# Performance work log

Hardware: AMD Instinct MI355X
Metric: run time of the kernel (lower is better)

## Reference

```python
import jax, jax.numpy as jnp
import numpy as np

N, D, H, O = 8192, 1024, 4096, 1024   # tokens, input_dim, hidden_dim, output_dim
E, K, CAP = 8, 2, 4096                # num_experts, top_k, expert_capacity


def setup_inputs() -> dict:
    key = jax.random.key(0)
    ks = jax.random.split(key, 7)
    sd = 0.02
    return {
        "x": jax.random.normal(ks[0], (N, D), jnp.float32),
        "gate_W": jax.random.normal(ks[1], (E, D), jnp.float32) * sd,
        "gate_b": jnp.zeros((E,), jnp.float32),
        "W1": jax.random.normal(ks[2], (E, D, H), jnp.float32) * sd,
        "b1": jnp.zeros((E, H), jnp.float32),
        "W2": jax.random.normal(ks[3], (E, H, O), jnp.float32) * sd,
        "b2": jnp.zeros((E, O), jnp.float32),
    }


def reference(x, gate_W, gate_b, W1, b1, W2, b2):
    n = x.shape[0]
    # --- gating ---
    logits = x @ gate_W.T + gate_b                      # [N, E]
    probs = jax.nn.softmax(logits, axis=-1)
    topk_probs, topk_idx = jax.lax.top_k(probs, K)      # [N, K]

    # --- aux losses (training mode) ---
    importance = probs.sum(0)                           # [E]
    importance_loss = jnp.var(importance, ddof=1) / (E ** 2)  # torch.var is unbiased
    mask = jnp.zeros((n, E), bool).at[jnp.arange(n)[:, None], topk_idx].set(True)
    routing_probs = probs * mask
    expert_usage = mask.astype(probs.dtype).mean(0)
    routing_weights = routing_probs.mean(0)
    load_balance_loss = E * (expert_usage * routing_weights).sum()
    aux_loss = importance_loss + load_balance_loss

    # --- capacity-constrained dispatch (matches torch flat-order truncation) ---
    flat_idx = topk_idx.reshape(-1)                     # [N*K] expert of each assignment
    flat_probs = topk_probs.reshape(-1)                 # [N*K]
    sample_idx = jnp.repeat(jnp.arange(n), K)           # [N*K] token of each assignment
    onehot = (flat_idx[:, None] == jnp.arange(E)[None, :])          # [N*K, E]
    pos = (jnp.cumsum(onehot, axis=0) * onehot).sum(-1) - 1         # slot within expert
    keep = pos < CAP                                    # torch keeps first CAP in flat order
    slot = jnp.where(keep, flat_idx * CAP + pos, E * CAP)           # dropped -> padding slot
    disp_sample = jnp.zeros(E * CAP + 1, jnp.int32).at[slot].set(sample_idx.astype(jnp.int32))
    disp_w = jnp.zeros(E * CAP + 1, x.dtype).at[slot].set(flat_probs)
    tok = disp_sample[: E * CAP]                        # [E*CAP] source token per slot

    # --- grouped expert MLP ---
    xe = x[tok].reshape(E, CAP, D)                      # gather into [E, CAP, D]
    h = jax.nn.relu(jnp.einsum('ecd,edh->ech', xe, W1) + b1[:, None, :])
    y = jnp.einsum('ech,eho->eco', h, W2) + b2[:, None, :]

    # --- weighted scatter-combine (unfilled slots have weight 0) ---
    w = disp_w[: E * CAP].reshape(E, CAP, 1)
    out = jnp.zeros((n, O), x.dtype).at[tok].add((y * w).reshape(E * CAP, O))
    return out, aux_loss
```

## Files before the change

kernel.cpp:

```cpp
#include <hip/hip_runtime.h>

#define N_TOK 8192
#define DIM   1024
#define HID   4096
#define OUTD  1024
#define NE    8
#define CAPE  4096

typedef _Float16 f16;
typedef f16  f16x8 __attribute__((ext_vector_type(8)));
typedef f16  f16x4 __attribute__((ext_vector_type(4)));
typedef float f32x4 __attribute__((ext_vector_type(4)));

__device__ __forceinline__ void gload16(const void* g, void* l) {
  __builtin_amdgcn_global_load_lds(
      (const __attribute__((address_space(1))) void*)g,
      (__attribute__((address_space(3))) void*)l, 16, 0, 0);
}

__global__ void zero_ctrl(int* counts) {
  if (threadIdx.x < NE) counts[threadIdx.x] = 0;
}

__global__ __launch_bounds__(256) void zero_out(float4* __restrict__ p) {
  p[(size_t)blockIdx.x * 256 + threadIdx.x] = float4{0.f, 0.f, 0.f, 0.f};
}

__global__ __launch_bounds__(256) void transpose_cvt(
    const float* __restrict__ in, f16* __restrict__ out, int R, int C, int g0) {
  __shared__ float tile[32][33];
  const int ez = blockIdx.z;
  const int r0 = blockIdx.y * 32;
  const int c0 = blockIdx.x * 32;
  const float* ip = in  + (size_t)(g0 + ez) * R * C;
  f16*         op = out + (size_t)ez * R * C;
  const int tx = threadIdx.x;
  const int ty = threadIdx.y;
#pragma unroll
  for (int k = 0; k < 4; ++k) {
    int r = ty + k * 8;
    tile[r][tx] = ip[(size_t)(r0 + r) * C + c0 + tx];
  }
  __syncthreads();
#pragma unroll
  for (int k = 0; k < 4; ++k) {
    int r = ty + k * 8;
    op[(size_t)(c0 + r) * R + r0 + tx] = (f16)tile[tx][r];
  }
}

__global__ __launch_bounds__(256) void gate_kernel(
    const float* __restrict__ x, const float* __restrict__ gW,
    const float* __restrict__ gb, int* __restrict__ counts,
    int* __restrict__ tk_e, int* __restrict__ tk_pos, float* __restrict__ tk_w,
    float* __restrict__ blockImp, float* __restrict__ blockRw) {
  const int tid  = threadIdx.x;
  const int wave = tid >> 6;
  const int lane = tid & 63;
  const int t    = blockIdx.x * 4 + wave;

  float acc[NE];
#pragma unroll
  for (int e = 0; e < NE; ++e) acc[e] = 0.f;

  const float* xr = x + (size_t)t * DIM;
  for (int d = lane; d < DIM; d += 64) {
    float xv = xr[d];
#pragma unroll
    for (int e = 0; e < NE; ++e) acc[e] += xv * gW[e * DIM + d];
  }
#pragma unroll
  for (int off = 32; off; off >>= 1) {
#pragma unroll
    for (int e = 0; e < NE; ++e) acc[e] += __shfl_xor(acc[e], off);
  }
  float p[NE];
  float mx = -1e30f;
#pragma unroll
  for (int e = 0; e < NE; ++e) { p[e] = acc[e] + gb[e]; mx = fmaxf(mx, p[e]); }
  float s = 0.f;
#pragma unroll
  for (int e = 0; e < NE; ++e) { p[e] = expf(p[e] - mx); s += p[e]; }
  float inv = 1.f / s;
#pragma unroll
  for (int e = 0; e < NE; ++e) p[e] *= inv;

  int e0 = 0;
#pragma unroll
  for (int e = 1; e < NE; ++e) if (p[e] > p[e0]) e0 = e;
  int e1 = (e0 == 0) ? 1 : 0;
#pragma unroll
  for (int e = 0; e < NE; ++e) if (e != e0 && p[e] > p[e1]) e1 = e;

  __shared__ float simp[4][NE];
  __shared__ float srw[4][NE];
  if (lane == 0) {
    int p0 = atomicAdd(&counts[e0], 1);
    int p1 = atomicAdd(&counts[e1], 1);
    tk_e[t * 2]     = e0;  tk_e[t * 2 + 1]   = e1;
    tk_pos[t * 2]   = p0;  tk_pos[t * 2 + 1] = p1;
    tk_w[t * 2]     = p[e0]; tk_w[t * 2 + 1] = p[e1];
#pragma unroll
    for (int e = 0; e < NE; ++e) {
      simp[wave][e] = p[e];
      srw[wave][e]  = (e == e0) ? p[e0] : ((e == e1) ? p[e1] : 0.f);
    }
  }
  __syncthreads();
  if (tid < NE) {
    float si = 0.f, sr = 0.f;
#pragma unroll
    for (int w = 0; w < 4; ++w) { si += simp[w][tid]; sr += srw[w][tid]; }
    blockImp[blockIdx.x * NE + tid] = si;
    blockRw[blockIdx.x * NE + tid]  = sr;
  }
}

__global__ __launch_bounds__(256) void gather_x(
    const float* __restrict__ x, const int* __restrict__ tk_e,
    const int* __restrict__ tk_pos, const float* __restrict__ tk_w,
    f16* __restrict__ Xg, int* __restrict__ slot_tok,
    float* __restrict__ slot_w, int g0, int G) {
  const int i   = blockIdx.x;
  const int e   = tk_e[i];
  if (e < g0 || e >= g0 + G) return;
  const int pos = tk_pos[i];
  if (pos >= CAPE) return;
  const int t = i >> 1;
  if (threadIdx.x == 0) {
    slot_tok[e * CAPE + pos] = t;
    slot_w[e * CAPE + pos]   = tk_w[i];
  }
  const float4* src = (const float4*)(x + (size_t)t * DIM);
  f16* dst = Xg + ((size_t)((e - g0) * CAPE + pos)) * DIM;
  const int c = threadIdx.x;
  float4 v = src[c];
  f16x4 h;
  h.x = (f16)v.x; h.y = (f16)v.y; h.z = (f16)v.z; h.w = (f16)v.w;
  *(f16x4*)(dst + c * 4) = h;
}

__global__ __launch_bounds__(256) void gemm1_kernel(
    const f16* __restrict__ Xg, const f16* __restrict__ W1t,
    const float* __restrict__ b1, f16* __restrict__ Hb,
    const int* __restrict__ counts, int g0) {
  const int ez  = blockIdx.z;
  const int e   = g0 + ez;
  int cnt = counts[e]; if (cnt > CAPE) cnt = CAPE;
  const int brow = blockIdx.y;
  const int bcol = blockIdx.x;
  if (brow * 128 >= cnt) return;

  __shared__ f16 As[128 * 32];
  __shared__ f16 Bs[128 * 32];

  const int tid  = threadIdx.x;
  const int wave = tid >> 6, lane = tid & 63;
  const int wr = wave >> 1, wc = wave & 1;
  const int srow = tid >> 2;
  const int scol = (tid & 3) * 8;

  const f16* Ab = Xg  + ((size_t)ez * CAPE + brow * 128) * DIM;
  const f16* Bb = W1t + ((size_t)ez * HID  + bcol * 128) * DIM;

  f32x4 acc[4][4];
#pragma unroll
  for (int i = 0; i < 4; ++i)
#pragma unroll
    for (int j = 0; j < 4; ++j) acc[i][j] = (f32x4){0.f, 0.f, 0.f, 0.f};

  const int fr = lane & 15, fk = (lane >> 4) * 8;

  for (int kt = 0; kt < DIM / 32; ++kt) {
    const f16* Ak = Ab + kt * 32;
    const f16* Bk = Bb + kt * 32;
    gload16(Ak + (size_t)srow * DIM + scol,        As + wave * 512);
    gload16(Ak + (size_t)(srow + 64) * DIM + scol, As + 2048 + wave * 512);
    gload16(Bk + (size_t)srow * DIM + scol,        Bs + wave * 512);
    gload16(Bk + (size_t)(srow + 64) * DIM + scol, Bs + 2048 + wave * 512);
    __syncthreads();
    f16x8 af[4], bf[4];
#pragma unroll
    for (int i = 0; i < 4; ++i)
      af[i] = *(const f16x8*)&As[(wr * 64 + i * 16 + fr) * 32 + fk];
#pragma unroll
    for (int j = 0; j < 4; ++j)
      bf[j] = *(const f16x8*)&Bs[(wc * 64 + j * 16 + fr) * 32 + fk];
#pragma unroll
    for (int i = 0; i < 4; ++i)
#pragma unroll
      for (int j = 0; j < 4; ++j)
        acc[i][j] = __builtin_amdgcn_mfma_f32_16x16x32_f16(af[i], bf[j], acc[i][j], 0, 0, 0);
    __syncthreads();
  }

  const int rbase = (lane >> 4) * 4;
  const int crow0 = brow * 128 + wr * 64;
  const int ccol0 = bcol * 128 + wc * 64;
  f16* Cb = Hb + (size_t)ez * CAPE * HID;
#pragma unroll
  for (int j = 0; j < 4; ++j) {
    int col = ccol0 + j * 16 + fr;
    float bias = b1[e * HID + col];
#pragma unroll
    for (int i = 0; i < 4; ++i) {
#pragma unroll
      for (int r = 0; r < 4; ++r) {
        int row = crow0 + i * 16 + rbase + r;
        float v = acc[i][j][r] + bias;
        Cb[(size_t)row * HID + col] = (f16)(v > 0.f ? v : 0.f);
      }
    }
  }
}

__global__ __launch_bounds__(256) void gemm2_kernel(
    const f16* __restrict__ Hb, const f16* __restrict__ W2t,
    const float* __restrict__ b2, float* __restrict__ out,
    const int* __restrict__ slot_tok, const float* __restrict__ slot_w,
    const int* __restrict__ counts, int g0) {
  const int ez  = blockIdx.z;
  const int e   = g0 + ez;
  int cnt = counts[e]; if (cnt > CAPE) cnt = CAPE;
  const int brow = blockIdx.y;
  const int bcol = blockIdx.x;
  if (brow * 128 >= cnt) return;

  __shared__ f16 As[128 * 32];
  __shared__ f16 Bs[128 * 32];

  const int tid  = threadIdx.x;
  const int wave = tid >> 6, lane = tid & 63;
  const int wr = wave >> 1, wc = wave & 1;
  const int srow = tid >> 2;
  const int scol = (tid & 3) * 8;

  const f16* Ab = Hb  + ((size_t)ez * CAPE + brow * 128) * HID;
  const f16* Bb = W2t + ((size_t)ez * OUTD + bcol * 128) * HID;

  f32x4 acc[4][4];
#pragma unroll
  for (int i = 0; i < 4; ++i)
#pragma unroll
    for (int j = 0; j < 4; ++j) acc[i][j] = (f32x4){0.f, 0.f, 0.f, 0.f};

  const int fr = lane & 15, fk = (lane >> 4) * 8;

  for (int kt = 0; kt < HID / 32; ++kt) {
    const f16* Ak = Ab + kt * 32;
    const f16* Bk = Bb + kt * 32;
    gload16(Ak + (size_t)srow * HID + scol,        As + wave * 512);
    gload16(Ak + (size_t)(srow + 64) * HID + scol, As + 2048 + wave * 512);
    gload16(Bk + (size_t)srow * HID + scol,        Bs + wave * 512);
    gload16(Bk + (size_t)(srow + 64) * HID + scol, Bs + 2048 + wave * 512);
    __syncthreads();
    f16x8 af[4], bf[4];
#pragma unroll
    for (int i = 0; i < 4; ++i)
      af[i] = *(const f16x8*)&As[(wr * 64 + i * 16 + fr) * 32 + fk];
#pragma unroll
    for (int j = 0; j < 4; ++j)
      bf[j] = *(const f16x8*)&Bs[(wc * 64 + j * 16 + fr) * 32 + fk];
#pragma unroll
    for (int i = 0; i < 4; ++i)
#pragma unroll
      for (int j = 0; j < 4; ++j)
        acc[i][j] = __builtin_amdgcn_mfma_f32_16x16x32_f16(af[i], bf[j], acc[i][j], 0, 0, 0);
    __syncthreads();
  }

  const int rbase = (lane >> 4) * 4;
  const int crow0 = brow * 128 + wr * 64;
  const int ccol0 = bcol * 128 + wc * 64;

  int   tok[4][4];
  float twt[4][4];
#pragma unroll
  for (int i = 0; i < 4; ++i) {
#pragma unroll
    for (int r = 0; r < 4; ++r) {
      int row = crow0 + i * 16 + rbase + r;
      if (row < cnt) {
        tok[i][r] = slot_tok[(size_t)e * CAPE + row];
        twt[i][r] = slot_w[(size_t)e * CAPE + row];
      } else {
        tok[i][r] = -1;
        twt[i][r] = 0.f;
      }
    }
  }

#pragma unroll
  for (int j = 0; j < 4; ++j) {
    int col = ccol0 + j * 16 + fr;
    float bias = b2[e * OUTD + col];
#pragma unroll
    for (int i = 0; i < 4; ++i) {
#pragma unroll
      for (int r = 0; r < 4; ++r) {
        if (tok[i][r] >= 0) {
          float v = twt[i][r] * (acc[i][j][r] + bias);
          atomicAdd(&out[(size_t)tok[i][r] * OUTD + col], v);
        }
      }
    }
  }
}

__global__ void aux_kernel(const float* __restrict__ blockImp,
                           const float* __restrict__ blockRw,
                           const int* __restrict__ counts,
                           float* __restrict__ out_aux) {
  const int lane = threadIdx.x;
  const int e   = lane >> 3;
  const int idx = lane & 7;
  double imp = 0.0, rw = 0.0;
  for (int b = idx; b < N_TOK / 4; b += 8) {
    imp += (double)blockImp[b * NE + e];
    rw  += (double)blockRw[b * NE + e];
  }
#pragma unroll
  for (int off = 1; off < 8; off <<= 1) {
    imp += __shfl_xor(imp, off);
    rw  += __shfl_xor(rw, off);
  }
  __shared__ double simp[NE], srw[NE];
  if (idx == 0) { simp[e] = imp; srw[e] = rw; }
  __syncthreads();
  if (lane == 0) {
    double mean = 0.0;
    for (int i = 0; i < NE; ++i) mean += simp[i];
    mean /= NE;
    double var = 0.0;
    for (int i = 0; i < NE; ++i) { double d = simp[i] - mean; var += d * d; }
    var /= (NE - 1);
    double il = var / (NE * NE);
    double lb = 0.0;
    for (int i = 0; i < NE; ++i)
      lb += ((double)counts[i] / N_TOK) * (srw[i] / N_TOK);
    lb *= NE;
    out_aux[0] = (float)(il + lb);
  }
}

extern "C" void kernel_launch(void* const* d_in, const int* in_sizes, int n_in,
                              void* d_out, int out_size, void* d_ws, size_t ws_size,
                              hipStream_t stream) {
  const float* x   = (const float*)d_in[0];
  const float* gW  = (const float*)d_in[1];
  const float* gb  = (const float*)d_in[2];
  const float* W1  = (const float*)d_in[3];
  const float* b1  = (const float*)d_in[4];
  const float* W2  = (const float*)d_in[5];
  const float* b2  = (const float*)d_in[6];
  float* out = (float*)d_out;

  char* ws = (char*)d_ws;
  size_t off = 0;
  int* counts   = (int*)(ws + off); off += 256;
  int* tk_e     = (int*)(ws + off); off += (size_t)N_TOK * 2 * 4;
  int* tk_pos   = (int*)(ws + off); off += (size_t)N_TOK * 2 * 4;
  float* tk_w   = (float*)(ws + off); off += (size_t)N_TOK * 2 * 4;
  int* slot_tok = (int*)(ws + off); off += (size_t)NE * CAPE * 4;
  float* slot_w = (float*)(ws + off); off += (size_t)NE * CAPE * 4;
  float* blockImp = (float*)(ws + off); off += (size_t)(N_TOK / 4) * NE * 4;
  float* blockRw  = (float*)(ws + off); off += (size_t)(N_TOK / 4) * NE * 4;
  off = (off + 255) & ~(size_t)255;

  const size_t w1t_pe = (size_t)HID  * DIM * 2;
  const size_t w2t_pe = (size_t)OUTD * HID * 2;
  const size_t xg_pe  = (size_t)CAPE * DIM * 2;
  const size_t hb_pe  = (size_t)CAPE * HID * 2;
  const size_t per_e  = w1t_pe + w2t_pe + xg_pe + hb_pe;

  int G = 1;
  for (int g = NE; g >= 1; g >>= 1) {
    if (off + (size_t)g * per_e <= ws_size) { G = g; break; }
  }

  f16* W1t = (f16*)(ws + off); off += (size_t)G * w1t_pe;
  f16* W2t = (f16*)(ws + off); off += (size_t)G * w2t_pe;
  f16* Xg  = (f16*)(ws + off); off += (size_t)G * xg_pe;
  f16* Hb  = (f16*)(ws + off);

  zero_ctrl<<<1, 64, 0, stream>>>(counts);
  zero_out<<<(N_TOK * OUTD / 4) / 256, 256, 0, stream>>>((float4*)out);

  gate_kernel<<<N_TOK / 4, 256, 0, stream>>>(x, gW, gb, counts, tk_e, tk_pos, tk_w,
                                             blockImp, blockRw);

  for (int g0 = 0; g0 < NE; g0 += G) {
    transpose_cvt<<<dim3(HID / 32, DIM / 32, G), dim3(32, 8), 0, stream>>>(
        W1, W1t, DIM, HID, g0);
    transpose_cvt<<<dim3(OUTD / 32, HID / 32, G), dim3(32, 8), 0, stream>>>(
        W2, W2t, HID, OUTD, g0);
    gather_x<<<N_TOK * 2, 256, 0, stream>>>(x, tk_e, tk_pos, tk_w, Xg,
                                            slot_tok, slot_w, g0, G);
    gemm1_kernel<<<dim3(HID / 128, CAPE / 128, G), 256, 0, stream>>>(
        Xg, W1t, b1, Hb, counts, g0);
    gemm2_kernel<<<dim3(OUTD / 128, CAPE / 128, G), 256, 0, stream>>>(
        Hb, W2t, b2, out, slot_tok, slot_w, counts, g0);
  }

  aux_kernel<<<1, 64, 0, stream>>>(blockImp, blockRw, counts, out + (size_t)N_TOK * OUTD);
}
```

Baseline: 1.213 ms.

## Replace atomic scatter-combine with fp16 expert output buffer and per-token gather

gemm2 now writes each expert's biased output to an fp16 buffer Yb and no longer does weighted float atomicAdds into the output. A new out_gather kernel reads the two routed rows per token, applies the gate weights and writes the output once. That removes the zero-fill kernel and atomic contention, at the cost of an extra fp16 write and read of the expert outputs and some precision loss. The weight transpose tiles also grow from 32x32 to 64x64 with a 64x4 thread block.

```diff
diff --git a/kernel.cpp b/kernel.cpp
--- a/kernel.cpp
+++ b/kernel.cpp
@@ -22,30 +22,26 @@
   if (threadIdx.x < NE) counts[threadIdx.x] = 0;
 }
 
-__global__ __launch_bounds__(256) void zero_out(float4* __restrict__ p) {
-  p[(size_t)blockIdx.x * 256 + threadIdx.x] = float4{0.f, 0.f, 0.f, 0.f};
-}
-
 __global__ __launch_bounds__(256) void transpose_cvt(
     const float* __restrict__ in, f16* __restrict__ out, int R, int C, int g0) {
-  __shared__ float tile[32][33];
+  __shared__ float tile[64][65];
   const int ez = blockIdx.z;
-  const int r0 = blockIdx.y * 32;
-  const int c0 = blockIdx.x * 32;
+  const int r0 = blockIdx.y * 64;
+  const int c0 = blockIdx.x * 64;
   const float* ip = in  + (size_t)(g0 + ez) * R * C;
   f16*         op = out + (size_t)ez * R * C;
   const int tx = threadIdx.x;
   const int ty = threadIdx.y;
 #pragma unroll
-  for (int k = 0; k < 4; ++k) {
-    int r = ty + k * 8;
+  for (int k = 0; k < 16; ++k) {
+    int r = ty + k * 4;
     tile[r][tx] = ip[(size_t)(r0 + r) * C + c0 + tx];
   }
   __syncthreads();
 #pragma unroll
-  for (int k = 0; k < 4; ++k) {
-    int r = ty + k * 8;
-    op[(size_t)(c0 + r) * R + r0 + tx] = (f16)tile[tx][r];
+  for (int k = 0; k < 16; ++k) {
+    int cc = ty + k * 4;
+    op[(size_t)(c0 + cc) * R + r0 + tx] = (f16)tile[tx][cc];
   }
 }
 
@@ -118,19 +114,13 @@
 
 __global__ __launch_bounds__(256) void gather_x(
     const float* __restrict__ x, const int* __restrict__ tk_e,
-    const int* __restrict__ tk_pos, const float* __restrict__ tk_w,
-    f16* __restrict__ Xg, int* __restrict__ slot_tok,
-    float* __restrict__ slot_w, int g0, int G) {
+    const int* __restrict__ tk_pos, f16* __restrict__ Xg, int g0, int G) {
   const int i   = blockIdx.x;
   const int e   = tk_e[i];
   if (e < g0 || e >= g0 + G) return;
   const int pos = tk_pos[i];
   if (pos >= CAPE) return;
   const int t = i >> 1;
-  if (threadIdx.x == 0) {
-    slot_tok[e * CAPE + pos] = t;
-    slot_w[e * CAPE + pos]   = tk_w[i];
-  }
   const float4* src = (const float4*)(x + (size_t)t * DIM);
   f16* dst = Xg + ((size_t)((e - g0) * CAPE + pos)) * DIM;
   const int c = threadIdx.x;
@@ -216,8 +206,7 @@
 
 __global__ __launch_bounds__(256) void gemm2_kernel(
     const f16* __restrict__ Hb, const f16* __restrict__ W2t,
-    const float* __restrict__ b2, float* __restrict__ out,
-    const int* __restrict__ slot_tok, const float* __restrict__ slot_w,
+    const float* __restrict__ b2, f16* __restrict__ Yb,
     const int* __restrict__ counts, int g0) {
   const int ez  = blockIdx.z;
   const int e   = g0 + ez;
@@ -272,24 +261,7 @@
   const int rbase = (lane >> 4) * 4;
   const int crow0 = brow * 128 + wr * 64;
   const int ccol0 = bcol * 128 + wc * 64;
-
-  int   tok[4][4];
-  float twt[4][4];
-#pragma unroll
-  for (int i = 0; i < 4; ++i) {
-#pragma unroll
-    for (int r = 0; r < 4; ++r) {
-      int row = crow0 + i * 16 + rbase + r;
-      if (row < cnt) {
-        tok[i][r] = slot_tok[(size_t)e * CAPE + row];
-        twt[i][r] = slot_w[(size_t)e * CAPE + row];
-      } else {
-        tok[i][r] = -1;
-        twt[i][r] = 0.f;
-      }
-    }
-  }
-
+  f16* Cb = Yb + (size_t)e * CAPE * OUTD;
 #pragma unroll
   for (int j = 0; j < 4; ++j) {
     int col = ccol0 + j * 16 + fr;
@@ -298,13 +270,34 @@
     for (int i = 0; i < 4; ++i) {
 #pragma unroll
       for (int r = 0; r < 4; ++r) {
-        if (tok[i][r] >= 0) {
-          float v = twt[i][r] * (acc[i][j][r] + bias);
-          atomicAdd(&out[(size_t)tok[i][r] * OUTD + col], v);
-        }
+        int row = crow0 + i * 16 + rbase + r;
+        Cb[(size_t)row * OUTD + col] = (f16)(acc[i][j][r] + bias);
       }
     }
   }
+}
+
+__global__ __launch_bounds__(256) void out_gather(
+    const f16* __restrict__ Yb, const int* __restrict__ tk_e,
+    const int* __restrict__ tk_pos, const float* __restrict__ tk_w,
+    float* __restrict__ out) {
+  const int t = blockIdx.x;
+  const int e0 = tk_e[t * 2],     e1 = tk_e[t * 2 + 1];
+  const int p0 = tk_pos[t * 2],   p1 = tk_pos[t * 2 + 1];
+  const float w0 = tk_w[t * 2],   w1 = tk_w[t * 2 + 1];
+  const int c = threadIdx.x;
+  float4 r = {0.f, 0.f, 0.f, 0.f};
+  if (p0 < CAPE) {
+    f16x4 y = *(const f16x4*)(Yb + ((size_t)(e0 * CAPE + p0)) * OUTD + c * 4);
+    r.x += w0 * (float)y.x; r.y += w0 * (float)y.y;
+    r.z += w0 * (float)y.z; r.w += w0 * (float)y.w;
+  }
+  if (p1 < CAPE) {
+    f16x4 y = *(const f16x4*)(Yb + ((size_t)(e1 * CAPE + p1)) * OUTD + c * 4);
+    r.x += w1 * (float)y.x; r.y += w1 * (float)y.y;
+    r.z += w1 * (float)y.z; r.w += w1 * (float)y.w;
+  }
+  ((float4*)(out + (size_t)t * OUTD))[c] = r;
 }
 
 __global__ void aux_kernel(const float* __restrict__ blockImp,
@@ -361,11 +354,11 @@
   int* tk_e     = (int*)(ws + off); off += (size_t)N_TOK * 2 * 4;
   int* tk_pos   = (int*)(ws + off); off += (size_t)N_TOK * 2 * 4;
   float* tk_w   = (float*)(ws + off); off += (size_t)N_TOK * 2 * 4;
-  int* slot_tok = (int*)(ws + off); off += (size_t)NE * CAPE * 4;
-  float* slot_w = (float*)(ws + off); off += (size_t)NE * CAPE * 4;
   float* blockImp = (float*)(ws + off); off += (size_t)(N_TOK / 4) * NE * 4;
   float* blockRw  = (float*)(ws + off); off += (size_t)(N_TOK / 4) * NE * 4;
   off = (off + 255) & ~(size_t)255;
+
+  f16* Yb = (f16*)(ws + off); off += (size_t)NE * CAPE * OUTD * 2;
 
   const size_t w1t_pe = (size_t)HID  * DIM * 2;
   const size_t w2t_pe = (size_t)OUTD * HID * 2;
@@ -384,23 +377,23 @@
   f16* Hb  = (f16*)(ws + off);
 
   zero_ctrl<<<1, 64, 0, stream>>>(counts);
-  zero_out<<<(N_TOK * OUTD / 4) / 256, 256, 0, stream>>>((float4*)out);
 
   gate_kernel<<<N_TOK / 4, 256, 0, stream>>>(x, gW, gb, counts, tk_e, tk_pos, tk_w,
                                              blockImp, blockRw);
 
   for (int g0 = 0; g0 < NE; g0 += G) {
-    transpose_cvt<<<dim3(HID / 32, DIM / 32, G), dim3(32, 8), 0, stream>>>(
+    transpose_cvt<<<dim3(HID / 64, DIM / 64, G), dim3(64, 4), 0, stream>>>(
         W1, W1t, DIM, HID, g0);
-    transpose_cvt<<<dim3(OUTD / 32, HID / 32, G), dim3(32, 8), 0, stream>>>(
+    transpose_cvt<<<dim3(OUTD / 64, HID / 64, G), dim3(64, 4), 0, stream>>>(
         W2, W2t, HID, OUTD, g0);
-    gather_x<<<N_TOK * 2, 256, 0, stream>>>(x, tk_e, tk_pos, tk_w, Xg,
-                                            slot_tok, slot_w, g0, G);
+    gather_x<<<N_TOK * 2, 256, 0, stream>>>(x, tk_e, tk_pos, Xg, g0, G);
     gemm1_kernel<<<dim3(HID / 128, CAPE / 128, G), 256, 0, stream>>>(
         Xg, W1t, b1, Hb, counts, g0);
     gemm2_kernel<<<dim3(OUTD / 128, CAPE / 128, G), 256, 0, stream>>>(
-        Hb, W2t, b2, out, slot_tok, slot_w, counts, g0);
-  }
+        Hb, W2t, b2, Yb, counts, g0);
+  }
+
+  out_gather<<<N_TOK, 256, 0, stream>>>(Yb, tk_e, tk_pos, tk_w, out);
 
   aux_kernel<<<1, 64, 0, stream>>>(blockImp, blockRw, counts, out + (size_t)N_TOK * OUTD);
 }
```

After: 1.066 ms. -12.1%, faster.
